# Kernel tuning notes

Hardware: AMD Instinct MI355X
Metric: run time of the kernel (lower is better)

The kernel has to match this reference:

```python
import jax, jax.numpy as jnp
import numpy as np

NEG_BIG = -9.0e15  # matches torch zero_vec constant


def setup_inputs() -> dict:
    key = jax.random.key(0)
    k1, k2, k3, k4, k5 = jax.random.split(key, 5)
    B, N, D_IN, D_HID, D_OUT = 4, 4096, 128, 64, 128
    h = jax.random.normal(k1, (B, N, D_IN), dtype=jnp.float32)
    adj = jax.random.randint(k2, (N, N), 0, 2, dtype=jnp.int32)
    Ws = jax.random.normal(k3, (D_IN, D_HID), dtype=jnp.float32) * (1.414 / np.sqrt(D_IN))
    Wt = jax.random.normal(k4, (D_IN, D_HID), dtype=jnp.float32) * (1.414 / np.sqrt(D_IN))
    Wc = jax.random.normal(k5, (D_IN, D_OUT), dtype=jnp.float32) * np.sqrt(2.0 / D_IN)
    return {"h": h, "adj": adj, "Ws": Ws, "Wt": Wt, "Wc": Wc}


def reference(h, adj, Ws, Wt, Wc):
    # h: [B,N,D_in], adj: [N,N] broadcast over batch
    Whs = jnp.matmul(h, Ws)                     # [B,N,H]
    Wht = jnp.matmul(h, Wt)                     # [B,N,H]
    e = jnp.einsum('bnh,bmh->bnm', Whs, Wht)    # [B,N,N] dense scores
    z = jnp.where(adj > 0, e, NEG_BIG)          # adjacency mask
    alpha = jax.nn.softmax(z, axis=-1)          # [B,N,N]
    Whc = jnp.matmul(h, Wc)                     # [B,N,D_out]
    h_prime = jnp.matmul(alpha, Whc)            # [B,N,D_out]
    return h_prime
```

## Files before the change

kernel.cpp:

```cpp
#include <hip/hip_runtime.h>
#include <hip/hip_bf16.h>

#define NTOK 4096
#define BATCH 4
#define DIN 128
#define DHID 64
#define DOUT 128
#define NWRD (NTOK / 32)
#define SPLIT 4
#define ITERS (NTOK / SPLIT / 64)
#define NEG_BIG -9.0e15f

typedef short short8 __attribute__((ext_vector_type(8)));
typedef short short4v __attribute__((ext_vector_type(4)));
typedef float floatx4 __attribute__((ext_vector_type(4)));

static __device__ __forceinline__ unsigned short f2bf(float f) {
    unsigned int u = __builtin_bit_cast(unsigned int, f);
    u = (u + 0x7fffu + ((u >> 16) & 1u)) >> 16;
    return (unsigned short)u;
}
static __device__ __forceinline__ float bf2f(unsigned short s) {
    unsigned int u = ((unsigned int)s) << 16;
    return __builtin_bit_cast(float, u);
}
static __device__ __forceinline__ unsigned int pk2(float lo, float hi) {
    unsigned int r;
    asm("v_cvt_pk_bf16_f32 %0, %1, %2" : "=v"(r) : "v"(lo), "v"(hi));
    return r;
}

static __device__ __forceinline__ floatx4 mfma16(short8 a, short8 b, floatx4 c) {
    return __builtin_amdgcn_mfma_f32_16x16x32_bf16(a, b, c, 0, 0, 0);
}

__global__ __launch_bounds__(256) void pack_adj_kernel(const int* __restrict__ adj,
                                                       unsigned int* __restrict__ bits) {
    int w = blockIdx.x * 256 + threadIdx.x;
    const int4* p = reinterpret_cast<const int4*>(adj) + (size_t)w * 8;
    unsigned int m = 0;
#pragma unroll
    for (int i = 0; i < 8; ++i) {
        int4 v = p[i];
        m |= (v.x > 0 ? 1u : 0u) << (4 * i + 0);
        m |= (v.y > 0 ? 1u : 0u) << (4 * i + 1);
        m |= (v.z > 0 ? 1u : 0u) << (4 * i + 2);
        m |= (v.w > 0 ? 1u : 0u) << (4 * i + 3);
    }
    bits[w] = m;
}

__global__ __launch_bounds__(256) void conv_w_kernel(const float* __restrict__ Ws,
                                                     const float* __restrict__ Wt,
                                                     const float* __restrict__ Wc,
                                                     unsigned short* __restrict__ WT_hi,
                                                     unsigned short* __restrict__ WT_lo) {
    int idx = blockIdx.x * 256 + threadIdx.x;
    int k = idx >> 8, col = idx & 255;
    float w;
    if (col < 64) w = Ws[k * DHID + col];
    else if (col < 128) w = Wt[k * DHID + (col - 64)];
    else w = Wc[k * DOUT + (col - 128)];
    unsigned short hi = f2bf(w);
    WT_hi[col * DIN + k] = hi;
    if (col < 128) WT_lo[col * DIN + k] = f2bf(w - bf2f(hi));
}

__global__ __launch_bounds__(256) void prep_kernel(const float* __restrict__ h,
                                                   const unsigned short* __restrict__ WT_hi,
                                                   const unsigned short* __restrict__ WT_lo,
                                                   unsigned short* __restrict__ Whs_hi,
                                                   unsigned short* __restrict__ Whs_lo,
                                                   unsigned short* __restrict__ Wht_hi,
                                                   unsigned short* __restrict__ Wht_lo,
                                                   unsigned short* __restrict__ WhcT) {
    int tid = threadIdx.x;
    int b = blockIdx.y;
    int w = tid >> 6, lane = tid & 63, lg = lane >> 4, lc = lane & 15;
    int n0 = blockIdx.x * 16;
    const float* hrow = h + (size_t)(b * NTOK + n0 + lc) * DIN;

    short8 ah[4], al[4];
#pragma unroll
    for (int ks = 0; ks < 4; ++ks) {
        float4 f0 = *reinterpret_cast<const float4*>(hrow + ks * 32 + lg * 8);
        float4 f1 = *reinterpret_cast<const float4*>(hrow + ks * 32 + lg * 8 + 4);
        float x[8] = {f0.x, f0.y, f0.z, f0.w, f1.x, f1.y, f1.z, f1.w};
        short8 hh, ll;
#pragma unroll
        for (int j = 0; j < 8; ++j) {
            unsigned short hb = f2bf(x[j]);
            hh[j] = (short)hb;
            ll[j] = (short)f2bf(x[j] - bf2f(hb));
        }
        ah[ks] = hh;
        al[ks] = ll;
    }

#pragma unroll
    for (int ci = 0; ci < 4; ++ci) {
        int ct = w * 4 + ci;
        int col = ct * 16 + lc;
        const unsigned short* bbase = WT_hi + (size_t)col * DIN;
        const unsigned short* lbase = WT_lo + (size_t)col * DIN;
        floatx4 acc = {0.f, 0.f, 0.f, 0.f};
#pragma unroll
        for (int ks = 0; ks < 4; ++ks) {
            short8 bh = *reinterpret_cast<const short8*>(bbase + ks * 32 + lg * 8);
            acc = mfma16(ah[ks], bh, acc);
            if (w < 2) {
                short8 bl = *reinterpret_cast<const short8*>(lbase + ks * 32 + lg * 8);
                acc = mfma16(ah[ks], bl, acc);
                acc = mfma16(al[ks], bh, acc);
            }
        }
        int nr = n0 + 4 * lg;
        if (w == 0) {
#pragma unroll
            for (int r = 0; r < 4; ++r) {
                float v = acc[r];
                unsigned short hb = f2bf(v);
                size_t o = (size_t)(b * NTOK + nr + r) * DHID + col;
                Whs_hi[o] = hb;
                Whs_lo[o] = f2bf(v - bf2f(hb));
            }
        } else if (w == 1) {
#pragma unroll
            for (int r = 0; r < 4; ++r) {
                float v = acc[r];
                unsigned short hb = f2bf(v);
                size_t o = (size_t)(b * NTOK + nr + r) * DHID + (col - 64);
                Wht_hi[o] = hb;
                Wht_lo[o] = f2bf(v - bf2f(hb));
            }
        } else {
            unsigned int p01 = (unsigned int)f2bf(acc[0]) | ((unsigned int)f2bf(acc[1]) << 16);
            unsigned int p23 = (unsigned int)f2bf(acc[2]) | ((unsigned int)f2bf(acc[3]) << 16);
            unsigned int* dst =
                reinterpret_cast<unsigned int*>(&WhcT[(size_t)(b * DOUT + col - 128) * NTOK + nr]);
            dst[0] = p01;
            dst[1] = p23;
        }
    }
}

__global__ __launch_bounds__(256, 4) void attn_kernel(const unsigned short* __restrict__ Whs_hi,
                                                      const unsigned short* __restrict__ Whs_lo,
                                                      const unsigned short* __restrict__ Wht_hi,
                                                      const unsigned short* __restrict__ Wht_lo,
                                                      const unsigned short* __restrict__ WhcT,
                                                      const unsigned int* __restrict__ bits,
                                                      unsigned short* __restrict__ po,
                                                      float* __restrict__ pm,
                                                      float* __restrict__ pl) {
    __shared__ unsigned short Kh_lds[64][72];
    __shared__ unsigned short Kl_lds[64][72];
    __shared__ unsigned short V_lds[128][72];

    int tid = threadIdx.x;
    int b = blockIdx.y;
    int split = blockIdx.z;
    int kbase = split * (NTOK / SPLIT);
    int lane = tid & 63, lg = lane >> 4, lc = lane & 15;
    int q0 = blockIdx.x * 64 + (tid >> 6) * 16;
    int n = q0 + lc;

    const unsigned short* qrowH = Whs_hi + (size_t)(b * NTOK + n) * DHID;
    const unsigned short* qrowL = Whs_lo + (size_t)(b * NTOK + n) * DHID;
    short8 qh0 = *reinterpret_cast<const short8*>(qrowH + lg * 8);
    short8 qh1 = *reinterpret_cast<const short8*>(qrowH + 32 + lg * 8);
    short8 ql0 = *reinterpret_cast<const short8*>(qrowL + lg * 8);
    short8 ql1 = *reinterpret_cast<const short8*>(qrowL + 32 + lg * 8);

    floatx4 o[8];
#pragma unroll
    for (int dt = 0; dt < 8; ++dt) o[dt] = (floatx4){0.f, 0.f, 0.f, 0.f};
    float m = NEG_BIG, l = 0.f;

    int kkey = tid >> 2, koff = (tid & 3) * 16;
    int vd = tid >> 1, va = tid & 1;

    short8 krH0, krH1, krL0, krL1, vr0, vr1, vr2, vr3;
    unsigned int mw0, mw1;

    {
        int kb = kbase;
        const unsigned short* ksrcH = Wht_hi + (size_t)(b * NTOK + kb + kkey) * DHID + koff;
        const unsigned short* ksrcL = Wht_lo + (size_t)(b * NTOK + kb + kkey) * DHID + koff;
        krH0 = *reinterpret_cast<const short8*>(ksrcH);
        krH1 = *reinterpret_cast<const short8*>(ksrcH + 8);
        krL0 = *reinterpret_cast<const short8*>(ksrcL);
        krL1 = *reinterpret_cast<const short8*>(ksrcL + 8);
        const unsigned short* vsrc = WhcT + (size_t)(b * DOUT + vd) * NTOK + kb + va * 32;
        vr0 = *reinterpret_cast<const short8*>(vsrc);
        vr1 = *reinterpret_cast<const short8*>(vsrc + 8);
        vr2 = *reinterpret_cast<const short8*>(vsrc + 16);
        vr3 = *reinterpret_cast<const short8*>(vsrc + 24);
        mw0 = bits[n * NWRD + (kb >> 5)];
        mw1 = bits[n * NWRD + (kb >> 5) + 1];
    }

    for (int it = 0; it < ITERS; ++it) {
        __syncthreads();
        *reinterpret_cast<short8*>(&Kh_lds[kkey][koff]) = krH0;
        *reinterpret_cast<short8*>(&Kh_lds[kkey][koff + 8]) = krH1;
        *reinterpret_cast<short8*>(&Kl_lds[kkey][koff]) = krL0;
        *reinterpret_cast<short8*>(&Kl_lds[kkey][koff + 8]) = krL1;
        {
            int sb = va * 32;
            const short8 vv[4] = {vr0, vr1, vr2, vr3};
#pragma unroll
            for (int j = 0; j < 4; ++j) {
                short4v lo4 = {vv[j][0], vv[j][1], vv[j][2], vv[j][3]};
                short4v hi4 = {vv[j][4], vv[j][5], vv[j][6], vv[j][7]};
                int s0 = sb + 16 * (j & 1) + 4 * (j >> 1);
                *reinterpret_cast<short4v*>(&V_lds[vd][s0]) = lo4;
                *reinterpret_cast<short4v*>(&V_lds[vd][s0 + 8]) = hi4;
            }
        }
        __syncthreads();

        floatx4 s[4];
        __builtin_amdgcn_s_setprio(1);
#pragma unroll
        for (int kc = 0; kc < 4; ++kc) {
            short8 kh0 = *reinterpret_cast<const short8*>(&Kh_lds[kc * 16 + lc][lg * 8]);
            short8 kh1 = *reinterpret_cast<const short8*>(&Kh_lds[kc * 16 + lc][32 + lg * 8]);
            short8 kl0 = *reinterpret_cast<const short8*>(&Kl_lds[kc * 16 + lc][lg * 8]);
            short8 kl1 = *reinterpret_cast<const short8*>(&Kl_lds[kc * 16 + lc][32 + lg * 8]);
            floatx4 acc = {0.f, 0.f, 0.f, 0.f};
            acc = mfma16(kh0, qh0, acc);
            acc = mfma16(kh1, qh1, acc);
            acc = mfma16(kh0, ql0, acc);
            acc = mfma16(kh1, ql1, acc);
            acc = mfma16(kl0, qh0, acc);
            acc = mfma16(kl1, qh1, acc);
            s[kc] = acc;
        }
        __builtin_amdgcn_s_setprio(0);

#pragma unroll
        for (int kc = 0; kc < 4; ++kc) {
            unsigned int word = (kc & 2) ? mw1 : mw0;
#pragma unroll
            for (int r = 0; r < 4; ++r) {
                int bit = 16 * (kc & 1) + 4 * lg + r;
                if (!((word >> bit) & 1u)) s[kc][r] = NEG_BIG;
            }
        }

        if (it + 1 < ITERS) {
            int kb = kbase + (it + 1) * 64;
            const unsigned short* ksrcH = Wht_hi + (size_t)(b * NTOK + kb + kkey) * DHID + koff;
            const unsigned short* ksrcL = Wht_lo + (size_t)(b * NTOK + kb + kkey) * DHID + koff;
            krH0 = *reinterpret_cast<const short8*>(ksrcH);
            krH1 = *reinterpret_cast<const short8*>(ksrcH + 8);
            krL0 = *reinterpret_cast<const short8*>(ksrcL);
            krL1 = *reinterpret_cast<const short8*>(ksrcL + 8);
            const unsigned short* vsrc = WhcT + (size_t)(b * DOUT + vd) * NTOK + kb + va * 32;
            vr0 = *reinterpret_cast<const short8*>(vsrc);
            vr1 = *reinterpret_cast<const short8*>(vsrc + 8);
            vr2 = *reinterpret_cast<const short8*>(vsrc + 16);
            vr3 = *reinterpret_cast<const short8*>(vsrc + 24);
            mw0 = bits[n * NWRD + (kb >> 5)];
            mw1 = bits[n * NWRD + (kb >> 5) + 1];
        }

        float vm = s[0][0];
#pragma unroll
        for (int kc = 0; kc < 4; ++kc)
#pragma unroll
            for (int r = 0; r < 4; ++r) vm = fmaxf(vm, s[kc][r]);
        vm = fmaxf(vm, __shfl_xor(vm, 16));
        vm = fmaxf(vm, __shfl_xor(vm, 32));
        float mn = fmaxf(m, vm);
        float sc = __expf(m - mn);
        m = mn;
        float rs = 0.f;
#pragma unroll
        for (int kc = 0; kc < 4; ++kc)
#pragma unroll
            for (int r = 0; r < 4; ++r) {
                float p = __expf(s[kc][r] - mn);
                s[kc][r] = p;
                rs += p;
            }
        rs += __shfl_xor(rs, 16);
        rs += __shfl_xor(rs, 32);
        l = l * sc + rs;

        float sc4[4];
#pragma unroll
        for (int r = 0; r < 4; ++r) sc4[r] = __shfl(sc, (lane & 48) + 4 * lg + r);
#pragma unroll
        for (int dt = 0; dt < 8; ++dt)
#pragma unroll
            for (int r = 0; r < 4; ++r) o[dt][r] *= sc4[r];

        unsigned int pw[8];
        pw[0] = pk2(s[0][0], s[0][1]); pw[1] = pk2(s[0][2], s[0][3]);
        pw[2] = pk2(s[1][0], s[1][1]); pw[3] = pk2(s[1][2], s[1][3]);
        pw[4] = pk2(s[2][0], s[2][1]); pw[5] = pk2(s[2][2], s[2][3]);
        pw[6] = pk2(s[3][0], s[3][1]); pw[7] = pk2(s[3][2], s[3][3]);
        short8 pa0 = __builtin_bit_cast(short8, *reinterpret_cast<uint4*>(&pw[0]));
        short8 pa1 = __builtin_bit_cast(short8, *reinterpret_cast<uint4*>(&pw[4]));

        __builtin_amdgcn_s_setprio(1);
#pragma unroll
        for (int dt = 0; dt < 8; ++dt) {
            short8 vf0 = *reinterpret_cast<const short8*>(&V_lds[dt * 16 + lc][lg * 8]);
            o[dt] = mfma16(pa0, vf0, o[dt]);
        }
#pragma unroll
        for (int dt = 0; dt < 8; ++dt) {
            short8 vf1 = *reinterpret_cast<const short8*>(&V_lds[dt * 16 + lc][32 + lg * 8]);
            o[dt] = mfma16(pa1, vf1, o[dt]);
        }
        __builtin_amdgcn_s_setprio(0);
    }

    float m4[4], l4[4];
#pragma unroll
    for (int r = 0; r < 4; ++r) {
        int src = (lane & 48) + 4 * lg + r;
        m4[r] = __shfl(m, src);
        l4[r] = __shfl(l, src);
    }
#pragma unroll
    for (int r = 0; r < 4; ++r) {
        size_t row = (size_t)(split * BATCH + b) * NTOK + q0 + 4 * lg + r;
        unsigned short* prow = po + row * DOUT;
#pragma unroll
        for (int dt = 0; dt < 8; ++dt) prow[dt * 16 + lc] = f2bf(o[dt][r]);
        if (lc == 0) {
            pm[row] = m4[r];
            pl[row] = l4[r];
        }
    }
}

__global__ __launch_bounds__(256) void merge_kernel(const unsigned short* __restrict__ po,
                                                    const float* __restrict__ pm,
                                                    const float* __restrict__ pl,
                                                    float* __restrict__ out) {
    int idx = blockIdx.x * 256 + threadIdx.x;
    int d = idx & (DOUT - 1);
    size_t bn = (size_t)(idx >> 7);
    const size_t BN = (size_t)BATCH * NTOK;

    float ms[SPLIT];
#pragma unroll
    for (int s = 0; s < SPLIT; ++s) ms[s] = pm[s * BN + bn];
    float M = ms[0];
#pragma unroll
    for (int s = 1; s < SPLIT; ++s) M = fmaxf(M, ms[s]);
    float L = 0.f, acc = 0.f;
#pragma unroll
    for (int s = 0; s < SPLIT; ++s) {
        float e = __expf(ms[s] - M);
        L += pl[s * BN + bn] * e;
        acc += bf2f(po[(s * BN + bn) * DOUT + d]) * e;
    }
    out[idx] = acc / L;
}

extern "C" void kernel_launch(void* const* d_in, const int* in_sizes, int n_in,
                              void* d_out, int out_size, void* d_ws, size_t ws_size,
                              hipStream_t stream) {
    const float* h   = (const float*)d_in[0];
    const int*   adj = (const int*)d_in[1];
    const float* Ws  = (const float*)d_in[2];
    const float* Wt  = (const float*)d_in[3];
    const float* Wc  = (const float*)d_in[4];
    float* out = (float*)d_out;

    size_t nq = (size_t)BATCH * NTOK * DHID;
    unsigned short* Whs_hi = (unsigned short*)d_ws;
    unsigned short* Whs_lo = Whs_hi + nq;
    unsigned short* Wht_hi = Whs_lo + nq;
    unsigned short* Wht_lo = Wht_hi + nq;
    unsigned short* WhcT   = Wht_lo + nq;
    unsigned int*   bits   = (unsigned int*)(WhcT + (size_t)BATCH * DOUT * NTOK);
    unsigned short* WT_hi  = (unsigned short*)(bits + (size_t)NTOK * NWRD);
    unsigned short* WT_lo  = WT_hi + 256 * DIN;
    unsigned short* po     = WT_lo + 128 * DIN;
    float*          pm     = (float*)(po + (size_t)SPLIT * BATCH * NTOK * DOUT);
    float*          pl     = pm + (size_t)SPLIT * BATCH * NTOK;

    pack_adj_kernel<<<dim3(NTOK * NWRD / 256), dim3(256), 0, stream>>>(adj, bits);
    conv_w_kernel<<<dim3(128), dim3(256), 0, stream>>>(Ws, Wt, Wc, WT_hi, WT_lo);
    prep_kernel<<<dim3(NTOK / 16, BATCH), dim3(256), 0, stream>>>(
        h, WT_hi, WT_lo, Whs_hi, Whs_lo, Wht_hi, Wht_lo, WhcT);
    attn_kernel<<<dim3(NTOK / 64, BATCH, SPLIT), dim3(256), 0, stream>>>(
        Whs_hi, Whs_lo, Wht_hi, Wht_lo, WhcT, bits, po, pm, pl);
    merge_kernel<<<dim3(BATCH * NTOK * DOUT / 256), dim3(256), 0, stream>>>(po, pm, pl, out);
}
```

Measured before the change: 222.0 us.

## Process two query tiles per wave to reuse K/V LDS loads

Each wave now handles 32 query rows as two 16-row groups instead of 16, so every K and V fragment read from LDS feeds two MFMA chains. This halves the number of blocks and the K/V global-to-LDS traffic per query row. Launch bounds drop to 2 waves per SIMD to make room for the doubled accumulators. The V transpose store into LDS also changes from eight 4-short stores to four 8-short stores built with shufflevector. The grid shrinks to 512 blocks, which lowers parallelism and occupancy.

```diff
diff --git a/kernel.cpp b/kernel.cpp
--- a/kernel.cpp
+++ b/kernel.cpp
@@ -12,7 +12,6 @@
 #define NEG_BIG -9.0e15f
 
 typedef short short8 __attribute__((ext_vector_type(8)));
-typedef short short4v __attribute__((ext_vector_type(4)));
 typedef float floatx4 __attribute__((ext_vector_type(4)));
 
 static __device__ __forceinline__ unsigned short f2bf(float f) {
@@ -144,7 +143,7 @@
     }
 }
 
-__global__ __launch_bounds__(256, 4) void attn_kernel(const unsigned short* __restrict__ Whs_hi,
+__global__ __launch_bounds__(256, 2) void attn_kernel(const unsigned short* __restrict__ Whs_hi,
                                                       const unsigned short* __restrict__ Whs_lo,
                                                       const unsigned short* __restrict__ Wht_hi,
                                                       const unsigned short* __restrict__ Wht_lo,
@@ -162,26 +161,35 @@
     int split = blockIdx.z;
     int kbase = split * (NTOK / SPLIT);
     int lane = tid & 63, lg = lane >> 4, lc = lane & 15;
-    int q0 = blockIdx.x * 64 + (tid >> 6) * 16;
-    int n = q0 + lc;
-
-    const unsigned short* qrowH = Whs_hi + (size_t)(b * NTOK + n) * DHID;
-    const unsigned short* qrowL = Whs_lo + (size_t)(b * NTOK + n) * DHID;
-    short8 qh0 = *reinterpret_cast<const short8*>(qrowH + lg * 8);
-    short8 qh1 = *reinterpret_cast<const short8*>(qrowH + 32 + lg * 8);
-    short8 ql0 = *reinterpret_cast<const short8*>(qrowL + lg * 8);
-    short8 ql1 = *reinterpret_cast<const short8*>(qrowL + 32 + lg * 8);
-
-    floatx4 o[8];
-#pragma unroll
-    for (int dt = 0; dt < 8; ++dt) o[dt] = (floatx4){0.f, 0.f, 0.f, 0.f};
-    float m = NEG_BIG, l = 0.f;
+    int q0 = blockIdx.x * 128 + (tid >> 6) * 32;
+    int nA = q0 + lc, nB = q0 + 16 + lc;
+
+    const unsigned short* qAH = Whs_hi + (size_t)(b * NTOK + nA) * DHID;
+    const unsigned short* qAL = Whs_lo + (size_t)(b * NTOK + nA) * DHID;
+    const unsigned short* qBH = Whs_hi + (size_t)(b * NTOK + nB) * DHID;
+    const unsigned short* qBL = Whs_lo + (size_t)(b * NTOK + nB) * DHID;
+    short8 qAh0 = *reinterpret_cast<const short8*>(qAH + lg * 8);
+    short8 qAh1 = *reinterpret_cast<const short8*>(qAH + 32 + lg * 8);
+    short8 qAl0 = *reinterpret_cast<const short8*>(qAL + lg * 8);
+    short8 qAl1 = *reinterpret_cast<const short8*>(qAL + 32 + lg * 8);
+    short8 qBh0 = *reinterpret_cast<const short8*>(qBH + lg * 8);
+    short8 qBh1 = *reinterpret_cast<const short8*>(qBH + 32 + lg * 8);
+    short8 qBl0 = *reinterpret_cast<const short8*>(qBL + lg * 8);
+    short8 qBl1 = *reinterpret_cast<const short8*>(qBL + 32 + lg * 8);
+
+    floatx4 o0[8], o1[8];
+#pragma unroll
+    for (int dt = 0; dt < 8; ++dt) {
+        o0[dt] = (floatx4){0.f, 0.f, 0.f, 0.f};
+        o1[dt] = (floatx4){0.f, 0.f, 0.f, 0.f};
+    }
+    float mA = NEG_BIG, lA = 0.f, mB = NEG_BIG, lB = 0.f;
 
     int kkey = tid >> 2, koff = (tid & 3) * 16;
     int vd = tid >> 1, va = tid & 1;
 
     short8 krH0, krH1, krL0, krL1, vr0, vr1, vr2, vr3;
-    unsigned int mw0, mw1;
+    unsigned int mwA0, mwA1, mwB0, mwB1;
 
     {
         int kb = kbase;
@@ -196,8 +204,10 @@
         vr1 = *reinterpret_cast<const short8*>(vsrc + 8);
         vr2 = *reinterpret_cast<const short8*>(vsrc + 16);
         vr3 = *reinterpret_cast<const short8*>(vsrc + 24);
-        mw0 = bits[n * NWRD + (kb >> 5)];
-        mw1 = bits[n * NWRD + (kb >> 5) + 1];
+        mwA0 = bits[nA * NWRD + (kb >> 5)];
+        mwA1 = bits[nA * NWRD + (kb >> 5) + 1];
+        mwB0 = bits[nB * NWRD + (kb >> 5)];
+        mwB1 = bits[nB * NWRD + (kb >> 5) + 1];
     }
 
     for (int it = 0; it < ITERS; ++it) {
@@ -208,19 +218,18 @@
         *reinterpret_cast<short8*>(&Kl_lds[kkey][koff + 8]) = krL1;
         {
             int sb = va * 32;
-            const short8 vv[4] = {vr0, vr1, vr2, vr3};
-#pragma unroll
-            for (int j = 0; j < 4; ++j) {
-                short4v lo4 = {vv[j][0], vv[j][1], vv[j][2], vv[j][3]};
-                short4v hi4 = {vv[j][4], vv[j][5], vv[j][6], vv[j][7]};
-                int s0 = sb + 16 * (j & 1) + 4 * (j >> 1);
-                *reinterpret_cast<short4v*>(&V_lds[vd][s0]) = lo4;
-                *reinterpret_cast<short4v*>(&V_lds[vd][s0 + 8]) = hi4;
-            }
+            short8 w00 = __builtin_shufflevector(vr0, vr2, 0, 1, 2, 3, 8, 9, 10, 11);
+            short8 w01 = __builtin_shufflevector(vr0, vr2, 4, 5, 6, 7, 12, 13, 14, 15);
+            short8 w10 = __builtin_shufflevector(vr1, vr3, 0, 1, 2, 3, 8, 9, 10, 11);
+            short8 w11 = __builtin_shufflevector(vr1, vr3, 4, 5, 6, 7, 12, 13, 14, 15);
+            *reinterpret_cast<short8*>(&V_lds[vd][sb]) = w00;
+            *reinterpret_cast<short8*>(&V_lds[vd][sb + 8]) = w01;
+            *reinterpret_cast<short8*>(&V_lds[vd][sb + 16]) = w10;
+            *reinterpret_cast<short8*>(&V_lds[vd][sb + 24]) = w11;
         }
         __syncthreads();
 
-        floatx4 s[4];
+        floatx4 s0[4], s1[4];
         __builtin_amdgcn_s_setprio(1);
 #pragma unroll
         for (int kc = 0; kc < 4; ++kc) {
@@ -228,24 +237,34 @@
             short8 kh1 = *reinterpret_cast<const short8*>(&Kh_lds[kc * 16 + lc][32 + lg * 8]);
             short8 kl0 = *reinterpret_cast<const short8*>(&Kl_lds[kc * 16 + lc][lg * 8]);
             short8 kl1 = *reinterpret_cast<const short8*>(&Kl_lds[kc * 16 + lc][32 + lg * 8]);
-            floatx4 acc = {0.f, 0.f, 0.f, 0.f};
-            acc = mfma16(kh0, qh0, acc);
-            acc = mfma16(kh1, qh1, acc);
-            acc = mfma16(kh0, ql0, acc);
-            acc = mfma16(kh1, ql1, acc);
-            acc = mfma16(kl0, qh0, acc);
-            acc = mfma16(kl1, qh1, acc);
-            s[kc] = acc;
+            floatx4 a0 = {0.f, 0.f, 0.f, 0.f};
+            a0 = mfma16(kh0, qAh0, a0);
+            a0 = mfma16(kh1, qAh1, a0);
+            a0 = mfma16(kh0, qAl0, a0);
+            a0 = mfma16(kh1, qAl1, a0);
+            a0 = mfma16(kl0, qAh0, a0);
+            a0 = mfma16(kl1, qAh1, a0);
+            s0[kc] = a0;
+            floatx4 a1 = {0.f, 0.f, 0.f, 0.f};
+            a1 = mfma16(kh0, qBh0, a1);
+            a1 = mfma16(kh1, qBh1, a1);
+            a1 = mfma16(kh0, qBl0, a1);
+            a1 = mfma16(kh1, qBl1, a1);
+            a1 = mfma16(kl0, qBh0, a1);
+            a1 = mfma16(kl1, qBh1, a1);
+            s1[kc] = a1;
         }
         __builtin_amdgcn_s_setprio(0);
 
 #pragma unroll
         for (int kc = 0; kc < 4; ++kc) {
-            unsigned int word = (kc & 2) ? mw1 : mw0;
+            unsigned int wA = (kc & 2) ? mwA1 : mwA0;
+            unsigned int wB = (kc & 2) ? mwB1 : mwB0;
 #pragma unroll
             for (int r = 0; r < 4; ++r) {
                 int bit = 16 * (kc & 1) + 4 * lg + r;
-                if (!((word >> bit) & 1u)) s[kc][r] = NEG_BIG;
+                if (!((wA >> bit) & 1u)) s0[kc][r] = NEG_BIG;
+                if (!((wB >> bit) & 1u)) s1[kc][r] = NEG_BIG;
             }
         }
 
@@ -262,79 +281,143 @@
             vr1 = *reinterpret_cast<const short8*>(vsrc + 8);
             vr2 = *reinterpret_cast<const short8*>(vsrc + 16);
             vr3 = *reinterpret_cast<const short8*>(vsrc + 24);
-            mw0 = bits[n * NWRD + (kb >> 5)];
-            mw1 = bits[n * NWRD + (kb >> 5) + 1];
-        }
-
-        float vm = s[0][0];
-#pragma unroll
-        for (int kc = 0; kc < 4; ++kc)
-#pragma unroll
-            for (int r = 0; r < 4; ++r) vm = fmaxf(vm, s[kc][r]);
-        vm = fmaxf(vm, __shfl_xor(vm, 16));
-        vm = fmaxf(vm, __shfl_xor(vm, 32));
-        float mn = fmaxf(m, vm);
-        float sc = __expf(m - mn);
-        m = mn;
-        float rs = 0.f;
-#pragma unroll
-        for (int kc = 0; kc < 4; ++kc)
-#pragma unroll
-            for (int r = 0; r < 4; ++r) {
-                float p = __expf(s[kc][r] - mn);
-                s[kc][r] = p;
-                rs += p;
-            }
-        rs += __shfl_xor(rs, 16);
-        rs += __shfl_xor(rs, 32);
-        l = l * sc + rs;
-
-        float sc4[4];
-#pragma unroll
-        for (int r = 0; r < 4; ++r) sc4[r] = __shfl(sc, (lane & 48) + 4 * lg + r);
-#pragma unroll
-        for (int dt = 0; dt < 8; ++dt)
-#pragma unroll
-            for (int r = 0; r < 4; ++r) o[dt][r] *= sc4[r];
+            mwA0 = bits[nA * NWRD + (kb >> 5)];
+            mwA1 = bits[nA * NWRD + (kb >> 5) + 1];
+            mwB0 = bits[nB * NWRD + (kb >> 5)];
+            mwB1 = bits[nB * NWRD + (kb >> 5) + 1];
+        }
+
+        float scA, scB;
+        {
+            float vm = s0[0][0];
+#pragma unroll
+            for (int kc = 0; kc < 4; ++kc)
+#pragma unroll
+                for (int r = 0; r < 4; ++r) vm = fmaxf(vm, s0[kc][r]);
+            vm = fmaxf(vm, __shfl_xor(vm, 16));
+            vm = fmaxf(vm, __shfl_xor(vm, 32));
+            float mn = fmaxf(mA, vm);
+            scA = __expf(mA - mn);
+            mA = mn;
+            float rs = 0.f;
+#pragma unroll
+            for (int kc = 0; kc < 4; ++kc)
+#pragma unroll
+                for (int r = 0; r < 4; ++r) {
+                    float p = __expf(s0[kc][r] - mn);
+                    s0[kc][r] = p;
+                    rs += p;
+                }
+            rs += __shfl_xor(rs, 16);
+            rs += __shfl_xor(rs, 32);
+            lA = lA * scA + rs;
+        }
+        {
+            float vm = s1[0][0];
+#pragma unroll
+            for (int kc = 0; kc < 4; ++kc)
+#pragma unroll
+                for (int r = 0; r < 4; ++r) vm = fmaxf(vm, s1[kc][r]);
+            vm = fmaxf(vm, __shfl_xor(vm, 16));
+            vm = fmaxf(vm, __shfl_xor(vm, 32));
+            float mn = fmaxf(mB, vm);
+            scB = __expf(mB - mn);
+            mB = mn;
+            float rs = 0.f;
+#pragma unroll
+            for (int kc = 0; kc < 4; ++kc)
+#pragma unroll
+                for (int r = 0; r < 4; ++r) {
+                    float p = __expf(s1[kc][r] - mn);
+                    s1[kc][r] = p;
+                    rs += p;
+                }
+            rs += __shfl_xor(rs, 16);
+            rs += __shfl_xor(rs, 32);
+            lB = lB * scB + rs;
+        }
+
+        {
+            float sc4[4];
+#pragma unroll
+            for (int r = 0; r < 4; ++r) sc4[r] = __shfl(scA, (lane & 48) + 4 * lg + r);
+#pragma unroll
+            for (int dt = 0; dt < 8; ++dt)
+#pragma unroll
+                for (int r = 0; r < 4; ++r) o0[dt][r] *= sc4[r];
+#pragma unroll
+            for (int r = 0; r < 4; ++r) sc4[r] = __shfl(scB, (lane & 48) + 4 * lg + r);
+#pragma unroll
+            for (int dt = 0; dt < 8; ++dt)
+#pragma unroll
+                for (int r = 0; r < 4; ++r) o1[dt][r] *= sc4[r];
+        }
 
         unsigned int pw[8];
-        pw[0] = pk2(s[0][0], s[0][1]); pw[1] = pk2(s[0][2], s[0][3]);
-        pw[2] = pk2(s[1][0], s[1][1]); pw[3] = pk2(s[1][2], s[1][3]);
-        pw[4] = pk2(s[2][0], s[2][1]); pw[5] = pk2(s[2][2], s[2][3]);
-        pw[6] = pk2(s[3][0], s[3][1]); pw[7] = pk2(s[3][2], s[3][3]);
-        short8 pa0 = __builtin_bit_cast(short8, *reinterpret_cast<uint4*>(&pw[0]));
-        short8 pa1 = __builtin_bit_cast(short8, *reinterpret_cast<uint4*>(&pw[4]));
+        pw[0] = pk2(s0[0][0], s0[0][1]); pw[1] = pk2(s0[0][2], s0[0][3]);
+        pw[2] = pk2(s0[1][0], s0[1][1]); pw[3] = pk2(s0[1][2], s0[1][3]);
+        pw[4] = pk2(s0[2][0], s0[2][1]); pw[5] = pk2(s0[2][2], s0[2][3]);
+        pw[6] = pk2(s0[3][0], s0[3][1]); pw[7] = pk2(s0[3][2], s0[3][3]);
+        short8 paA0 = __builtin_bit_cast(short8, *reinterpret_cast<uint4*>(&pw[0]));
+        short8 paA1 = __builtin_bit_cast(short8, *reinterpret_cast<uint4*>(&pw[4]));
+        pw[0] = pk2(s1[0][0], s1[0][1]); pw[1] = pk2(s1[0][2], s1[0][3]);
+        pw[2] = pk2(s1[1][0], s1[1][1]); pw[3] = pk2(s1[1][2], s1[1][3]);
+        pw[4] = pk2(s1[2][0], s1[2][1]); pw[5] = pk2(s1[2][2], s1[2][3]);
+        pw[6] = pk2(s1[3][0], s1[3][1]); pw[7] = pk2(s1[3][2], s1[3][3]);
+        short8 paB0 = __builtin_bit_cast(short8, *reinterpret_cast<uint4*>(&pw[0]));
+        short8 paB1 = __builtin_bit_cast(short8, *reinterpret_cast<uint4*>(&pw[4]));
 
         __builtin_amdgcn_s_setprio(1);
 #pragma unroll
         for (int dt = 0; dt < 8; ++dt) {
             short8 vf0 = *reinterpret_cast<const short8*>(&V_lds[dt * 16 + lc][lg * 8]);
-            o[dt] = mfma16(pa0, vf0, o[dt]);
+            o0[dt] = mfma16(paA0, vf0, o0[dt]);
+            o1[dt] = mfma16(paB0, vf0, o1[dt]);
         }
 #pragma unroll
         for (int dt = 0; dt < 8; ++dt) {
             short8 vf1 = *reinterpret_cast<const short8*>(&V_lds[dt * 16 + lc][32 + lg * 8]);
-            o[dt] = mfma16(pa1, vf1, o[dt]);
+            o0[dt] = mfma16(paA1, vf1, o0[dt]);
+            o1[dt] = mfma16(paB1, vf1, o1[dt]);
         }
         __builtin_amdgcn_s_setprio(0);
     }
 
-    float m4[4], l4[4];
-#pragma unroll
-    for (int r = 0; r < 4; ++r) {
-        int src = (lane & 48) + 4 * lg + r;
-        m4[r] = __shfl(m, src);
-        l4[r] = __shfl(l, src);
-    }
-#pragma unroll
-    for (int r = 0; r < 4; ++r) {
-        size_t row = (size_t)(split * BATCH + b) * NTOK + q0 + 4 * lg + r;
-        unsigned short* prow = po + row * DOUT;
-#pragma unroll
-        for (int dt = 0; dt < 8; ++dt) prow[dt * 16 + lc] = f2bf(o[dt][r]);
-        if (lc == 0) {
-            pm[row] = m4[r];
-            pl[row] = l4[r];
+    {
+        float m4[4], l4[4];
+#pragma unroll
+        for (int r = 0; r < 4; ++r) {
+            int src = (lane & 48) + 4 * lg + r;
+            m4[r] = __shfl(mA, src);
+            l4[r] = __shfl(lA, src);
+        }
+#pragma unroll
+        for (int r = 0; r < 4; ++r) {
+            size_t row = (size_t)(split * BATCH + b) * NTOK + q0 + 4 * lg + r;
+            unsigned short* prow = po + row * DOUT;
+#pragma unroll
+            for (int dt = 0; dt < 8; ++dt) prow[dt * 16 + lc] = f2bf(o0[dt][r]);
+            if (lc == 0) {
+                pm[row] = m4[r];
+                pl[row] = l4[r];
+            }
+        }
+#pragma unroll
+        for (int r = 0; r < 4; ++r) {
+            int src = (lane & 48) + 4 * lg + r;
+            m4[r] = __shfl(mB, src);
+            l4[r] = __shfl(lB, src);
+        }
+#pragma unroll
+        for (int r = 0; r < 4; ++r) {
+            size_t row = (size_t)(split * BATCH + b) * NTOK + q0 + 16 + 4 * lg + r;
+            unsigned short* prow = po + row * DOUT;
+#pragma unroll
+            for (int dt = 0; dt < 8; ++dt) prow[dt * 16 + lc] = f2bf(o1[dt][r]);
+            if (lc == 0) {
+                pm[row] = m4[r];
+                pl[row] = l4[r];
+            }
         }
     }
 }
@@ -391,7 +474,7 @@
     conv_w_kernel<<<dim3(128), dim3(256), 0, stream>>>(Ws, Wt, Wc, WT_hi, WT_lo);
     prep_kernel<<<dim3(NTOK / 16, BATCH), dim3(256), 0, stream>>>(
         h, WT_hi, WT_lo, Whs_hi, Whs_lo, Wht_hi, Wht_lo, WhcT);
-    attn_kernel<<<dim3(NTOK / 64, BATCH, SPLIT), dim3(256), 0, stream>>>(
+    attn_kernel<<<dim3(NTOK / 128, BATCH, SPLIT), dim3(256), 0, stream>>>(
         Whs_hi, Whs_lo, Wht_hi, Wht_lo, WhcT, bits, po, pm, pl);
     merge_kernel<<<dim3(BATCH * NTOK * DOUT / 256), dim3(256), 0, stream>>>(po, pm, pl, out);
 }
```

New measurement: 189.5 us. -14.6%, faster.
